# Performance work log

Measured on AMD Instinct MI355X. Metric: run time of the kernel, lower is better.

## Reference

```python
import jax, jax.numpy as jnp
import numpy as np

N = 100000
E = 1600000
IN_DIM, HID_DIM, OUT_DIM = 128, 128, 64


def setup_inputs() -> dict:
    key = jax.random.key(0)
    k1, k2, k3, k4, k5, k6 = jax.random.split(key, 6)
    x = jax.random.normal(k1, (N, IN_DIM), dtype=jnp.float32)
    edge_index = jax.random.randint(k2, (2, E), 0, N, dtype=jnp.int64)
    # Glorot-style scaled weights (PyG GCNConv: Linear without bias + separate bias)
    W1 = jax.random.normal(k3, (IN_DIM, HID_DIM), dtype=jnp.float32) / np.sqrt(IN_DIM)
    b1 = jnp.zeros((HID_DIM,), dtype=jnp.float32)
    W2 = jax.random.normal(k4, (HID_DIM, OUT_DIM), dtype=jnp.float32) / np.sqrt(HID_DIM)
    b2 = jnp.zeros((OUT_DIM,), dtype=jnp.float32)
    return {"x": x, "W1": W1, "b1": b1, "W2": W2, "b2": b2, "edge_index": edge_index}


def _gcn_norm(edge_index, num_nodes):
    """Add self-loops and compute symmetric normalization D^-1/2 A_hat D^-1/2."""
    loop = jnp.arange(num_nodes, dtype=edge_index.dtype)
    src = jnp.concatenate([edge_index[0], loop])  # [E + N]
    dst = jnp.concatenate([edge_index[1], loop])
    deg = jax.ops.segment_sum(jnp.ones_like(dst, dtype=jnp.float32), dst,
                              num_segments=num_nodes)
    deg_inv_sqrt = jnp.where(deg > 0, jax.lax.rsqrt(deg), 0.0)
    norm = deg_inv_sqrt[src] * deg_inv_sqrt[dst]  # [E + N]
    return src, dst, norm


def _gcn_conv(x, W, b, src, dst, norm, num_nodes):
    h = x @ W                                   # [N, out]  dense transform first
    msg = norm[:, None] * h[src]                # gather + scale over edges
    out = jax.ops.segment_sum(msg, dst, num_segments=num_nodes)  # scatter-add
    return out + b


def reference(x, W1, b1, W2, b2, edge_index):
    num_nodes = x.shape[0]
    src, dst, norm = _gcn_norm(edge_index, num_nodes)
    h = jax.nn.relu(_gcn_conv(x, W1, b1, src, dst, norm, num_nodes))
    out = _gcn_conv(h, W2, b2, src, dst, norm, num_nodes)
    return out
```

## Files before the change

### kernel.cpp

```cpp
#include <hip/hip_runtime.h>

#define NODES 100000
#define EDGES 1600000
#define CHUNK 8192
#define NCH 196
#define BSH 9
#define NBUCK 196

typedef unsigned int uint;
typedef unsigned short ushort;

__device__ __forceinline__ float bf2f(uint u) {
    union { uint i; float f; } c; c.i = u << 16; return c.f;
}
__device__ __forceinline__ ushort f2bf(float f) {
    union { float f; uint i; } c; c.f = f;
    uint r = c.i + 0x7fff + ((c.i >> 16) & 1);
    return (ushort)(r >> 16);
}


__global__ __launch_bounds__(256) void k_hist(const int* __restrict__ dst,
                                              int* __restrict__ hist) {
    __shared__ int h[NBUCK];
    const int t = threadIdx.x;
    if (t < NBUCK) h[t] = 0;
    __syncthreads();
    const int base = blockIdx.x * CHUNK;
    const int len = min(CHUNK, EDGES - base);
    for (int i = t; i < len; i += 256)
        atomicAdd(&h[dst[base + i] >> BSH], 1);
    __syncthreads();
    if (t < NBUCK) hist[blockIdx.x * NBUCK + t] = h[t];
}

__global__ void k_offsets(int* __restrict__ hist, int* __restrict__ bucketStart,
                          int* __restrict__ rowptr) {
    __shared__ int tot[NBUCK];
    __shared__ int bstart[NBUCK + 1];
    const int t = threadIdx.x;
    if (t < NBUCK) {
        int run = 0;
        for (int blk = 0; blk < NCH; ++blk) {
            int c = hist[blk * NBUCK + t];
            hist[blk * NBUCK + t] = run;
            run += c;
        }
        tot[t] = run;
    }
    __syncthreads();
    if (t == 0) {
        int acc = 0;
        for (int b = 0; b < NBUCK; ++b) { bstart[b] = acc; acc += tot[b]; }
        bstart[NBUCK] = acc;
        rowptr[NODES] = acc;
    }
    __syncthreads();
    if (t < NBUCK) {
        int bs = bstart[t];
        for (int blk = 0; blk < NCH; ++blk)
            hist[blk * NBUCK + t] += bs;
    }
    if (t <= NBUCK) bucketStart[t] = bstart[t];
}

__global__ __launch_bounds__(256) void k_bin(const int* __restrict__ src,
                                             const int* __restrict__ dst,
                                             const int* __restrict__ hist,
                                             uint* __restrict__ binned) {
    __shared__ int curs[NBUCK];
    const int t = threadIdx.x;
    if (t < NBUCK) curs[t] = hist[blockIdx.x * NBUCK + t];
    __syncthreads();
    const int base = blockIdx.x * CHUNK;
    const int len = min(CHUNK, EDGES - base);
    for (int i = t; i < len; i += 256) {
        int d = dst[base + i];
        int s = src[base + i];
        int pos = atomicAdd(&curs[d >> BSH], 1);
        binned[pos] = ((uint)(d & 511) << 17) | (uint)s;
    }
}

__global__ __launch_bounds__(256) void k_build(const uint* __restrict__ binned,
                                               const int* __restrict__ bucketStart,
                                               int* __restrict__ rowptr,
                                               float* __restrict__ dis,
                                               int* __restrict__ ssrc) {
    __shared__ int cnt[512];
    __shared__ int sh[256];
    const int t = threadIdx.x;
    const int b = blockIdx.x;
    const int eBase = bucketStart[b], eEnd = bucketStart[b + 1];
    const int nodeBase = b << BSH;
    const int nnode = min(512, NODES - nodeBase);
    cnt[t * 2] = 0; cnt[t * 2 + 1] = 0;
    __syncthreads();
    for (int i = eBase + t; i < eEnd; i += 256)
        atomicAdd(&cnt[binned[i] >> 17], 1);
    __syncthreads();
    const int c0 = cnt[t * 2], c1 = cnt[t * 2 + 1];
    const int sum = c0 + c1;
    sh[t] = sum; __syncthreads();
    for (int off = 1; off < 256; off <<= 1) {
        int add = (t >= off) ? sh[t - off] : 0;
        __syncthreads(); sh[t] += add; __syncthreads();
    }
    int excl = sh[t] - sum;
    const int ln0 = t * 2;
    if (ln0 < nnode) {
        rowptr[nodeBase + ln0] = eBase + excl;
        dis[nodeBase + ln0] = rsqrtf((float)(1 + c0));
    }
    int excl1 = excl + c0;
    if (ln0 + 1 < nnode) {
        rowptr[nodeBase + ln0 + 1] = eBase + excl1;
        dis[nodeBase + ln0 + 1] = rsqrtf((float)(1 + c1));
    }
    cnt[ln0] = excl; cnt[ln0 + 1] = excl1;
    __syncthreads();
    for (int i = eBase + t; i < eEnd; i += 256) {
        uint p = binned[i];
        int pos = atomicAdd(&cnt[p >> 17], 1);
        ssrc[eBase + pos] = (int)(p & 0x1FFFFu);
    }
}


__global__ __launch_bounds__(256) void k_gemm1(const float* __restrict__ x,
                                               const float* __restrict__ W1,
                                               ushort* __restrict__ hb) {
    __shared__ float wsh[128 * 128];
    __shared__ float xs[32 * 128];
    const int t = threadIdx.x;
    {
        const float4* Wv = (const float4*)W1;
        float4* Sv = (float4*)wsh;
#pragma unroll
        for (int i = 0; i < 16; ++i) Sv[i * 256 + t] = Wv[i * 256 + t];
    }
    const int row0 = blockIdx.x * 32;
    {
        const float4* Xv = (const float4*)(x + (size_t)row0 * 128);
        float4* Sv = (float4*)xs;
#pragma unroll
        for (int i = 0; i < 4; ++i) Sv[i * 256 + t] = Xv[i * 256 + t];
    }
    __syncthreads();
    const int c4 = (t & 31) * 4;
    const int r0 = (t >> 5) * 4;
    float4 a0{0,0,0,0}, a1{0,0,0,0}, a2{0,0,0,0}, a3{0,0,0,0};
#pragma unroll 4
    for (int k = 0; k < 128; ++k) {
        float4 w = *(const float4*)&wsh[k * 128 + c4];
        float x0 = xs[(r0 + 0) * 128 + k];
        float x1 = xs[(r0 + 1) * 128 + k];
        float x2 = xs[(r0 + 2) * 128 + k];
        float x3 = xs[(r0 + 3) * 128 + k];
        a0.x = fmaf(x0, w.x, a0.x); a0.y = fmaf(x0, w.y, a0.y);
        a0.z = fmaf(x0, w.z, a0.z); a0.w = fmaf(x0, w.w, a0.w);
        a1.x = fmaf(x1, w.x, a1.x); a1.y = fmaf(x1, w.y, a1.y);
        a1.z = fmaf(x1, w.z, a1.z); a1.w = fmaf(x1, w.w, a1.w);
        a2.x = fmaf(x2, w.x, a2.x); a2.y = fmaf(x2, w.y, a2.y);
        a2.z = fmaf(x2, w.z, a2.z); a2.w = fmaf(x2, w.w, a2.w);
        a3.x = fmaf(x3, w.x, a3.x); a3.y = fmaf(x3, w.y, a3.y);
        a3.z = fmaf(x3, w.z, a3.z); a3.w = fmaf(x3, w.w, a3.w);
    }
    size_t base = (size_t)(row0 + r0) * 128 + c4;
    ushort4 u;
    u.x = f2bf(a0.x); u.y = f2bf(a0.y); u.z = f2bf(a0.z); u.w = f2bf(a0.w);
    *(ushort4*)&hb[base] = u;
    u.x = f2bf(a1.x); u.y = f2bf(a1.y); u.z = f2bf(a1.z); u.w = f2bf(a1.w);
    *(ushort4*)&hb[base + 128] = u;
    u.x = f2bf(a2.x); u.y = f2bf(a2.y); u.z = f2bf(a2.z); u.w = f2bf(a2.w);
    *(ushort4*)&hb[base + 256] = u;
    u.x = f2bf(a3.x); u.y = f2bf(a3.y); u.z = f2bf(a3.z); u.w = f2bf(a3.w);
    *(ushort4*)&hb[base + 384] = u;
}

__global__ __launch_bounds__(256) void k_gemm2(const uint* __restrict__ ab,
                                               const float* __restrict__ W2,
                                               ushort* __restrict__ gb) {
    __shared__ float wsh[128 * 64];
    __shared__ float xs[32 * 132];
    const int t = threadIdx.x;
    {
        const float4* Wv = (const float4*)W2;
        float4* Sv = (float4*)wsh;
#pragma unroll
        for (int i = 0; i < 8; ++i) Sv[i * 256 + t] = Wv[i * 256 + t];
    }
    const int row0 = blockIdx.x * 32;
    {
        const uint4* Xv = (const uint4*)(ab + (size_t)row0 * 64);
#pragma unroll
        for (int i = 0; i < 2; ++i) {
            int f = i * 256 + t;
            uint4 vv = Xv[f];
            int row = f >> 4, col = (f & 15) * 8;
            float* d = &xs[row * 132 + col];
            d[0] = bf2f(vv.x & 0xffffu); d[1] = bf2f(vv.x >> 16);
            d[2] = bf2f(vv.y & 0xffffu); d[3] = bf2f(vv.y >> 16);
            d[4] = bf2f(vv.z & 0xffffu); d[5] = bf2f(vv.z >> 16);
            d[6] = bf2f(vv.w & 0xffffu); d[7] = bf2f(vv.w >> 16);
        }
    }
    __syncthreads();
    const int c4 = (t & 15) * 4;
    const int r0 = (t >> 4) * 2;
    float4 a0{0,0,0,0}, a1{0,0,0,0};
#pragma unroll 4
    for (int k = 0; k < 128; ++k) {
        float4 w = *(const float4*)&wsh[k * 64 + c4];
        float x0 = xs[(r0 + 0) * 132 + k];
        float x1 = xs[(r0 + 1) * 132 + k];
        a0.x = fmaf(x0, w.x, a0.x); a0.y = fmaf(x0, w.y, a0.y);
        a0.z = fmaf(x0, w.z, a0.z); a0.w = fmaf(x0, w.w, a0.w);
        a1.x = fmaf(x1, w.x, a1.x); a1.y = fmaf(x1, w.y, a1.y);
        a1.z = fmaf(x1, w.z, a1.z); a1.w = fmaf(x1, w.w, a1.w);
    }
    size_t base = (size_t)(row0 + r0) * 64 + c4;
    ushort4 u;
    u.x = f2bf(a0.x); u.y = f2bf(a0.y); u.z = f2bf(a0.z); u.w = f2bf(a0.w);
    *(ushort4*)&gb[base] = u;
    u.x = f2bf(a1.x); u.y = f2bf(a1.y); u.z = f2bf(a1.z); u.w = f2bf(a1.w);
    *(ushort4*)&gb[base + 64] = u;
}


__global__ void k_agg1(const int* __restrict__ rowptr, const int* __restrict__ ssrc,
                       const float* __restrict__ dis, const uint* __restrict__ hb,
                       const float* __restrict__ b1, uint* __restrict__ ab) {
    const int t = threadIdx.x;
    const int v = blockIdx.x * 4 + (t >> 6);
    const int j = t & 63;
    const float dv = dis[v];
    uint pv = hb[(size_t)v * 64 + j];
    float ax = dv * bf2f(pv & 0xffffu);
    float ay = dv * bf2f(pv >> 16);
    float bx = 0.f, by = 0.f;
    int e = rowptr[v];
    const int end = rowptr[v + 1];
    while (e < end) {
        int m = end - e; if (m > 64) m = 64;
        int s = 0; float dsv = 0.f;
        if (j < m) { s = ssrc[e + j]; dsv = dis[s]; }
        int i = 0;
        for (; i + 2 <= m; i += 2) {
            int s0 = __shfl(s, i), s1 = __shfl(s, i + 1);
            float d0 = __shfl(dsv, i), d1 = __shfl(dsv, i + 1);
            uint p0 = hb[(size_t)s0 * 64 + j];
            uint p1 = hb[(size_t)s1 * 64 + j];
            ax = fmaf(d0, bf2f(p0 & 0xffffu), ax);
            ay = fmaf(d0, bf2f(p0 >> 16), ay);
            bx = fmaf(d1, bf2f(p1 & 0xffffu), bx);
            by = fmaf(d1, bf2f(p1 >> 16), by);
        }
        if (i < m) {
            int s0 = __shfl(s, i); float d0 = __shfl(dsv, i);
            uint p0 = hb[(size_t)s0 * 64 + j];
            ax = fmaf(d0, bf2f(p0 & 0xffffu), ax);
            ay = fmaf(d0, bf2f(p0 >> 16), ay);
        }
        e += m;
    }
    float2 bb = ((const float2*)b1)[j];
    float ox = fmaxf(fmaf(dv, ax + bx, bb.x), 0.f);
    float oy = fmaxf(fmaf(dv, ay + by, bb.y), 0.f);
    ab[(size_t)v * 64 + j] = ((uint)f2bf(oy) << 16) | (uint)f2bf(ox);
}

__global__ void k_agg2(const int* __restrict__ rowptr, const int* __restrict__ ssrc,
                       const float* __restrict__ dis, const ushort* __restrict__ gb,
                       const float* __restrict__ b2, float* __restrict__ out) {
    const int t = threadIdx.x;
    const int v = blockIdx.x * 4 + (t >> 6);
    const int j = t & 63;
    const float dv = dis[v];
    float ax = dv * bf2f((uint)gb[(size_t)v * 64 + j]);
    float bx = 0.f;
    int e = rowptr[v];
    const int end = rowptr[v + 1];
    while (e < end) {
        int m = end - e; if (m > 64) m = 64;
        int s = 0; float dsv = 0.f;
        if (j < m) { s = ssrc[e + j]; dsv = dis[s]; }
        int i = 0;
        for (; i + 2 <= m; i += 2) {
            int s0 = __shfl(s, i), s1 = __shfl(s, i + 1);
            float d0 = __shfl(dsv, i), d1 = __shfl(dsv, i + 1);
            float g0 = bf2f((uint)gb[(size_t)s0 * 64 + j]);
            float g1 = bf2f((uint)gb[(size_t)s1 * 64 + j]);
            ax = fmaf(d0, g0, ax);
            bx = fmaf(d1, g1, bx);
        }
        if (i < m) {
            int s0 = __shfl(s, i); float d0 = __shfl(dsv, i);
            ax = fmaf(d0, bf2f((uint)gb[(size_t)s0 * 64 + j]), ax);
        }
        e += m;
    }
    out[(size_t)v * 64 + j] = fmaf(dv, ax + bx, b2[j]);
}


extern "C" void kernel_launch(void* const* d_in, const int* in_sizes, int n_in,
                              void* d_out, int out_size, void* d_ws, size_t ws_size,
                              hipStream_t stream) {
    const float* x  = (const float*)d_in[0];
    const float* W1 = (const float*)d_in[1];
    const float* b1 = (const float*)d_in[2];
    const float* W2 = (const float*)d_in[3];
    const float* b2 = (const float*)d_in[4];
    const int*   ei = (const int*)d_in[5];
    const int* src = ei;
    const int* dst = ei + EDGES;
    float* out = (float*)d_out;

    char* w = (char*)d_ws;
    int*    hist   = (int*)w;    w += (size_t)NCH * NBUCK * 4 + 256;
    int*    bstart = (int*)w;    w += 256 * 4;
    int*    rowptr = (int*)w;    w += 100004 * 4;
    float*  dis    = (float*)w;  w += 100000 * 4;
    uint*   binned = (uint*)w;   w += (size_t)EDGES * 4;
    int*    ssrc   = (int*)w;    w += (size_t)EDGES * 4;
    ushort* hb     = (ushort*)w; w += (size_t)NODES * 128 * 2;
    uint*   ab     = (uint*)w;   w += (size_t)NODES * 64 * 4;
    ushort* gb     = (ushort*)w; w += (size_t)NODES * 64 * 2;

    k_hist   <<<NCH, 256, 0, stream>>>(dst, hist);
    k_offsets<<<1, 256, 0, stream>>>(hist, bstart, rowptr);
    k_bin    <<<NCH, 256, 0, stream>>>(src, dst, hist, binned);
    k_build  <<<NBUCK, 256, 0, stream>>>(binned, bstart, rowptr, dis, ssrc);

    k_gemm1  <<<NODES / 32, 256, 0, stream>>>(x, W1, hb);
    k_agg1   <<<NODES / 4, 256, 0, stream>>>(rowptr, ssrc, dis, (const uint*)hb, b1, ab);
    k_gemm2  <<<NODES / 32, 256, 0, stream>>>(ab, W2, gb);
    k_agg2   <<<NODES / 4, 256, 0, stream>>>(rowptr, ssrc, dis, gb, b2, out);
}
```

Measured before the change: 404.2 us.

## Prescale GEMM outputs by source degree and split aggregation wavefronts across two edges

The GEMM epilogues now multiply each row by its deg^-1/2 before storing bf16. This removes the per-edge dis[s] gather and the FMA scale from both aggregation kernels. The aggregation kernels are also restructured so each half-wavefront handles a different edge with wider per-lane loads (uint2/uint). The halves are combined with a shuffle-xor at the end, and only half the lanes write output. In exchange, rounding to bf16 now happens after scaling and the output stores use half the lanes.

```diff
diff --git a/kernel.cpp b/kernel.cpp
--- a/kernel.cpp
+++ b/kernel.cpp
@@ -129,6 +129,7 @@
 
 __global__ __launch_bounds__(256) void k_gemm1(const float* __restrict__ x,
                                                const float* __restrict__ W1,
+                                               const float* __restrict__ dis,
                                                ushort* __restrict__ hb) {
     __shared__ float wsh[128 * 128];
     __shared__ float xs[32 * 128];
@@ -166,20 +167,23 @@
         a3.x = fmaf(x3, w.x, a3.x); a3.y = fmaf(x3, w.y, a3.y);
         a3.z = fmaf(x3, w.z, a3.z); a3.w = fmaf(x3, w.w, a3.w);
     }
+    const float d0 = dis[row0 + r0], d1 = dis[row0 + r0 + 1];
+    const float d2 = dis[row0 + r0 + 2], d3 = dis[row0 + r0 + 3];
     size_t base = (size_t)(row0 + r0) * 128 + c4;
     ushort4 u;
-    u.x = f2bf(a0.x); u.y = f2bf(a0.y); u.z = f2bf(a0.z); u.w = f2bf(a0.w);
+    u.x = f2bf(a0.x * d0); u.y = f2bf(a0.y * d0); u.z = f2bf(a0.z * d0); u.w = f2bf(a0.w * d0);
     *(ushort4*)&hb[base] = u;
-    u.x = f2bf(a1.x); u.y = f2bf(a1.y); u.z = f2bf(a1.z); u.w = f2bf(a1.w);
+    u.x = f2bf(a1.x * d1); u.y = f2bf(a1.y * d1); u.z = f2bf(a1.z * d1); u.w = f2bf(a1.w * d1);
     *(ushort4*)&hb[base + 128] = u;
-    u.x = f2bf(a2.x); u.y = f2bf(a2.y); u.z = f2bf(a2.z); u.w = f2bf(a2.w);
+    u.x = f2bf(a2.x * d2); u.y = f2bf(a2.y * d2); u.z = f2bf(a2.z * d2); u.w = f2bf(a2.w * d2);
     *(ushort4*)&hb[base + 256] = u;
-    u.x = f2bf(a3.x); u.y = f2bf(a3.y); u.z = f2bf(a3.z); u.w = f2bf(a3.w);
+    u.x = f2bf(a3.x * d3); u.y = f2bf(a3.y * d3); u.z = f2bf(a3.z * d3); u.w = f2bf(a3.w * d3);
     *(ushort4*)&hb[base + 384] = u;
 }
 
 __global__ __launch_bounds__(256) void k_gemm2(const uint* __restrict__ ab,
                                                const float* __restrict__ W2,
+                                               const float* __restrict__ dis,
                                                ushort* __restrict__ gb) {
     __shared__ float wsh[128 * 64];
     __shared__ float xs[32 * 132];
@@ -219,88 +223,136 @@
         a1.x = fmaf(x1, w.x, a1.x); a1.y = fmaf(x1, w.y, a1.y);
         a1.z = fmaf(x1, w.z, a1.z); a1.w = fmaf(x1, w.w, a1.w);
     }
+    const float d0 = dis[row0 + r0], d1 = dis[row0 + r0 + 1];
     size_t base = (size_t)(row0 + r0) * 64 + c4;
     ushort4 u;
-    u.x = f2bf(a0.x); u.y = f2bf(a0.y); u.z = f2bf(a0.z); u.w = f2bf(a0.w);
+    u.x = f2bf(a0.x * d0); u.y = f2bf(a0.y * d0); u.z = f2bf(a0.z * d0); u.w = f2bf(a0.w * d0);
     *(ushort4*)&gb[base] = u;
-    u.x = f2bf(a1.x); u.y = f2bf(a1.y); u.z = f2bf(a1.z); u.w = f2bf(a1.w);
+    u.x = f2bf(a1.x * d1); u.y = f2bf(a1.y * d1); u.z = f2bf(a1.z * d1); u.w = f2bf(a1.w * d1);
     *(ushort4*)&gb[base + 64] = u;
 }
 
 
 __global__ void k_agg1(const int* __restrict__ rowptr, const int* __restrict__ ssrc,
-                       const float* __restrict__ dis, const uint* __restrict__ hb,
-                       const float* __restrict__ b1, uint* __restrict__ ab) {
+                       const float* __restrict__ dis, const uint2* __restrict__ hb2,
+                       const float* __restrict__ b1, uint2* __restrict__ ab2) {
     const int t = threadIdx.x;
     const int v = blockIdx.x * 4 + (t >> 6);
-    const int j = t & 63;
-    const float dv = dis[v];
-    uint pv = hb[(size_t)v * 64 + j];
-    float ax = dv * bf2f(pv & 0xffffu);
-    float ay = dv * bf2f(pv >> 16);
-    float bx = 0.f, by = 0.f;
+    const int lane = t & 63;
+    const int half = lane >> 5;
+    const int q = lane & 31;
+    float4 accA = {0.f, 0.f, 0.f, 0.f}, accB = {0.f, 0.f, 0.f, 0.f};
+    if (half == 0) {
+        uint2 pv = hb2[(size_t)v * 32 + q];
+        accA.x = bf2f(pv.x & 0xffffu); accA.y = bf2f(pv.x >> 16);
+        accA.z = bf2f(pv.y & 0xffffu); accA.w = bf2f(pv.y >> 16);
+    }
     int e = rowptr[v];
     const int end = rowptr[v + 1];
     while (e < end) {
         int m = end - e; if (m > 64) m = 64;
-        int s = 0; float dsv = 0.f;
-        if (j < m) { s = ssrc[e + j]; dsv = dis[s]; }
+        int s = (lane < m) ? ssrc[e + lane] : 0;
         int i = 0;
-        for (; i + 2 <= m; i += 2) {
-            int s0 = __shfl(s, i), s1 = __shfl(s, i + 1);
-            float d0 = __shfl(dsv, i), d1 = __shfl(dsv, i + 1);
-            uint p0 = hb[(size_t)s0 * 64 + j];
-            uint p1 = hb[(size_t)s1 * 64 + j];
-            ax = fmaf(d0, bf2f(p0 & 0xffffu), ax);
-            ay = fmaf(d0, bf2f(p0 >> 16), ay);
-            bx = fmaf(d1, bf2f(p1 & 0xffffu), bx);
-            by = fmaf(d1, bf2f(p1 >> 16), by);
+        for (; i + 4 <= m; i += 4) {
+            int s0 = __shfl(s, i + half);
+            int s1 = __shfl(s, i + 2 + half);
+            uint2 p0 = hb2[(size_t)s0 * 32 + q];
+            uint2 p1 = hb2[(size_t)s1 * 32 + q];
+            accA.x += bf2f(p0.x & 0xffffu); accA.y += bf2f(p0.x >> 16);
+            accA.z += bf2f(p0.y & 0xffffu); accA.w += bf2f(p0.y >> 16);
+            accB.x += bf2f(p1.x & 0xffffu); accB.y += bf2f(p1.x >> 16);
+            accB.z += bf2f(p1.y & 0xffffu); accB.w += bf2f(p1.y >> 16);
+        }
+        if (i + 2 <= m) {
+            int s0 = __shfl(s, i + half);
+            uint2 p0 = hb2[(size_t)s0 * 32 + q];
+            accA.x += bf2f(p0.x & 0xffffu); accA.y += bf2f(p0.x >> 16);
+            accA.z += bf2f(p0.y & 0xffffu); accA.w += bf2f(p0.y >> 16);
+            i += 2;
         }
         if (i < m) {
-            int s0 = __shfl(s, i); float d0 = __shfl(dsv, i);
-            uint p0 = hb[(size_t)s0 * 64 + j];
-            ax = fmaf(d0, bf2f(p0 & 0xffffu), ax);
-            ay = fmaf(d0, bf2f(p0 >> 16), ay);
+            int s0 = __shfl(s, i);
+            uint2 p0 = hb2[(size_t)s0 * 32 + q];
+            if (half == 0) {
+                accA.x += bf2f(p0.x & 0xffffu); accA.y += bf2f(p0.x >> 16);
+                accA.z += bf2f(p0.y & 0xffffu); accA.w += bf2f(p0.y >> 16);
+            }
         }
         e += m;
     }
-    float2 bb = ((const float2*)b1)[j];
-    float ox = fmaxf(fmaf(dv, ax + bx, bb.x), 0.f);
-    float oy = fmaxf(fmaf(dv, ay + by, bb.y), 0.f);
-    ab[(size_t)v * 64 + j] = ((uint)f2bf(oy) << 16) | (uint)f2bf(ox);
+    float4 tot;
+    tot.x = accA.x + accB.x; tot.y = accA.y + accB.y;
+    tot.z = accA.z + accB.z; tot.w = accA.w + accB.w;
+    tot.x += __shfl_xor(tot.x, 32); tot.y += __shfl_xor(tot.y, 32);
+    tot.z += __shfl_xor(tot.z, 32); tot.w += __shfl_xor(tot.w, 32);
+    if (half == 0) {
+        const float dv = dis[v];
+        const float4 bb = ((const float4*)b1)[q];
+        float ox = fmaxf(fmaf(dv, tot.x, bb.x), 0.f);
+        float oy = fmaxf(fmaf(dv, tot.y, bb.y), 0.f);
+        float oz = fmaxf(fmaf(dv, tot.z, bb.z), 0.f);
+        float ow = fmaxf(fmaf(dv, tot.w, bb.w), 0.f);
+        uint2 o;
+        o.x = ((uint)f2bf(oy) << 16) | (uint)f2bf(ox);
+        o.y = ((uint)f2bf(ow) << 16) | (uint)f2bf(oz);
+        ab2[(size_t)v * 32 + q] = o;
+    }
 }
 
 __global__ void k_agg2(const int* __restrict__ rowptr, const int* __restrict__ ssrc,
-                       const float* __restrict__ dis, const ushort* __restrict__ gb,
+                       const float* __restrict__ dis, const uint* __restrict__ gbu,
                        const float* __restrict__ b2, float* __restrict__ out) {
     const int t = threadIdx.x;
     const int v = blockIdx.x * 4 + (t >> 6);
-    const int j = t & 63;
-    const float dv = dis[v];
-    float ax = dv * bf2f((uint)gb[(size_t)v * 64 + j]);
-    float bx = 0.f;
+    const int lane = t & 63;
+    const int half = lane >> 5;
+    const int q = lane & 31;
+    float2 accA = {0.f, 0.f}, accB = {0.f, 0.f};
+    if (half == 0) {
+        uint pv = gbu[(size_t)v * 32 + q];
+        accA.x = bf2f(pv & 0xffffu); accA.y = bf2f(pv >> 16);
+    }
     int e = rowptr[v];
     const int end = rowptr[v + 1];
     while (e < end) {
         int m = end - e; if (m > 64) m = 64;
-        int s = 0; float dsv = 0.f;
-        if (j < m) { s = ssrc[e + j]; dsv = dis[s]; }
+        int s = (lane < m) ? ssrc[e + lane] : 0;
         int i = 0;
-        for (; i + 2 <= m; i += 2) {
-            int s0 = __shfl(s, i), s1 = __shfl(s, i + 1);
-            float d0 = __shfl(dsv, i), d1 = __shfl(dsv, i + 1);
-            float g0 = bf2f((uint)gb[(size_t)s0 * 64 + j]);
-            float g1 = bf2f((uint)gb[(size_t)s1 * 64 + j]);
-            ax = fmaf(d0, g0, ax);
-            bx = fmaf(d1, g1, bx);
+        for (; i + 4 <= m; i += 4) {
+            int s0 = __shfl(s, i + half);
+            int s1 = __shfl(s, i + 2 + half);
+            uint p0 = gbu[(size_t)s0 * 32 + q];
+            uint p1 = gbu[(size_t)s1 * 32 + q];
+            accA.x += bf2f(p0 & 0xffffu); accA.y += bf2f(p0 >> 16);
+            accB.x += bf2f(p1 & 0xffffu); accB.y += bf2f(p1 >> 16);
+        }
+        if (i + 2 <= m) {
+            int s0 = __shfl(s, i + half);
+            uint p0 = gbu[(size_t)s0 * 32 + q];
+            accA.x += bf2f(p0 & 0xffffu); accA.y += bf2f(p0 >> 16);
+            i += 2;
         }
         if (i < m) {
-            int s0 = __shfl(s, i); float d0 = __shfl(dsv, i);
-            ax = fmaf(d0, bf2f((uint)gb[(size_t)s0 * 64 + j]), ax);
+            int s0 = __shfl(s, i);
+            uint p0 = gbu[(size_t)s0 * 32 + q];
+            if (half == 0) {
+                accA.x += bf2f(p0 & 0xffffu); accA.y += bf2f(p0 >> 16);
+            }
         }
         e += m;
     }
-    out[(size_t)v * 64 + j] = fmaf(dv, ax + bx, b2[j]);
+    float2 tot;
+    tot.x = accA.x + accB.x; tot.y = accA.y + accB.y;
+    tot.x += __shfl_xor(tot.x, 32);
+    tot.y += __shfl_xor(tot.y, 32);
+    if (half == 0) {
+        const float dv = dis[v];
+        const float2 bb = ((const float2*)b2)[q];
+        float2 o;
+        o.x = fmaf(dv, tot.x, bb.x);
+        o.y = fmaf(dv, tot.y, bb.y);
+        ((float2*)out)[(size_t)v * 32 + q] = o;
+    }
 }
 
 
@@ -321,7 +373,7 @@
     int*    hist   = (int*)w;    w += (size_t)NCH * NBUCK * 4 + 256;
     int*    bstart = (int*)w;    w += 256 * 4;
     int*    rowptr = (int*)w;    w += 100004 * 4;
-    float*  dis    = (float*)w;  w += 100000 * 4;
+    float*  dis    = (float*)w;  w += 100000 * 4 + 16;
     uint*   binned = (uint*)w;   w += (size_t)EDGES * 4;
     int*    ssrc   = (int*)w;    w += (size_t)EDGES * 4;
     ushort* hb     = (ushort*)w; w += (size_t)NODES * 128 * 2;
@@ -333,8 +385,8 @@
     k_bin    <<<NCH, 256, 0, stream>>>(src, dst, hist, binned);
     k_build  <<<NBUCK, 256, 0, stream>>>(binned, bstart, rowptr, dis, ssrc);
 
-    k_gemm1  <<<NODES / 32, 256, 0, stream>>>(x, W1, hb);
-    k_agg1   <<<NODES / 4, 256, 0, stream>>>(rowptr, ssrc, dis, (const uint*)hb, b1, ab);
-    k_gemm2  <<<NODES / 32, 256, 0, stream>>>(ab, W2, gb);
-    k_agg2   <<<NODES / 4, 256, 0, stream>>>(rowptr, ssrc, dis, gb, b2, out);
-}
+    k_gemm1  <<<NODES / 32, 256, 0, stream>>>(x, W1, dis, hb);
+    k_agg1   <<<NODES / 4, 256, 0, stream>>>(rowptr, ssrc, dis, (const uint2*)hb, b1, (uint2*)ab);
+    k_gemm2  <<<NODES / 32, 256, 0, stream>>>(ab, W2, dis, gb);
+    k_agg2   <<<NODES / 4, 256, 0, stream>>>(rowptr, ssrc, dis, (const uint*)gb, b2, out);
+}
```

Result: no change. 397.6 us (-1.6%).
